# Optimization experiments

Measured on AMD Instinct MI355X. Metric: run time of the kernel, lower is better.

## Reference

```python
import jax, jax.numpy as jnp
import numpy as np

H = 8
D_MODEL = 1024
D_K = D_MODEL // H
NEG = -1000000000.0


def layer_norm(x, a, b, eps=1e-06):
    # torch std: unbiased (ddof=1); module divides by (std + eps)
    mean = jnp.mean(x, axis=-1, keepdims=True)
    var = jnp.sum((x - mean) ** 2, axis=-1, keepdims=True) / (x.shape[-1] - 1)
    std = jnp.sqrt(var)
    return a * (x - mean) / (std + eps) + b


def setup_inputs() -> dict:
    key = jax.random.key(0)
    ks = jax.random.split(key, 12)
    B, S, D = 8, 1024, D_MODEL
    inp = {
        "query": jax.random.normal(ks[0], (B, S, D), jnp.float32),
        "value": jax.random.normal(ks[1], (B, S, D), jnp.float32),
        "key": jax.random.normal(ks[2], (B, S, D), jnp.float32),
        "mask": jax.random.randint(ks[3], (B, S), 0, 2, jnp.int32),
        "ln_a": jnp.ones((D,), jnp.float32),
        "ln_b": jnp.zeros((D,), jnp.float32),
        "wq": jax.random.normal(ks[4], (D, D), jnp.float32) * 0.02,
        "bq": jnp.zeros((D,), jnp.float32),
        "wk": jax.random.normal(ks[5], (D, D), jnp.float32) * 0.02,
        "bk": jnp.zeros((D,), jnp.float32),
        "wv": jax.random.normal(ks[6], (D, D), jnp.float32) * 0.02,
        "bv": jnp.zeros((D,), jnp.float32),
        "w_aoa": jax.random.normal(ks[7], (2 * D, 2 * D), jnp.float32) * 0.02,  # [out, in]
        "b_aoa": jnp.zeros((2 * D,), jnp.float32),
    }
    return inp


def reference(query, value, key, mask, ln_a, ln_b, wq, bq, wk, bk, wv, bv, w_aoa, b_aoa):
    B, S, D = query.shape
    # mask [B,S] -> [B,1,1,S]
    m = mask[:, None, None, :]
    # norm_q
    q = layer_norm(query, ln_a, ln_b)
    # QKV projections, split heads -> [B,H,S,Dk]
    def split_heads(x):
        return x.reshape(B, -1, H, D_K).transpose(0, 2, 1, 3)
    q_ = split_heads(q @ wq.T + bq)
    k_ = split_heads(key @ wk.T + bk)
    v_ = split_heads(value @ wv.T + bv)
    scores = jnp.einsum("bhqd,bhkd->bhqk", q_, k_) / jnp.sqrt(jnp.float32(D_K))
    scores = jnp.where(m == 0, NEG, scores)
    p = jax.nn.softmax(scores, axis=-1)
    x = jnp.einsum("bhqk,bhkd->bhqd", p, v_)
    x = x.transpose(0, 2, 1, 3).reshape(B, S, D)
    # AoA: concat with (normed) query, linear to 2D, GLU
    z = jnp.concatenate([x, q], axis=-1) @ w_aoa.T + b_aoa
    a, g = jnp.split(z, 2, axis=-1)
    return a * jax.nn.sigmoid(g)
```

## Files before the change

### kernel.cpp

```cpp
#include <hip/hip_runtime.h>

typedef __attribute__((ext_vector_type(8))) __bf16 bf16x8;
typedef __attribute__((ext_vector_type(4))) float f32x4;

__device__ __forceinline__ ushort f2b(float f) {
    uint u = __builtin_bit_cast(uint, f);
    u += 0x7fffu + ((u >> 16) & 1u);
    return (ushort)(u >> 16);
}
__device__ __forceinline__ float b2f(ushort h) {
    uint u = ((uint)h) << 16;
    return __builtin_bit_cast(float, u);
}

__global__ __launch_bounds__(256) void cast_kernel(const float* __restrict__ src,
                                                   ushort* __restrict__ dst) {
    size_t i = ((size_t)blockIdx.x * 256 + threadIdx.x) * 4;
    float4 v = *(const float4*)(src + i);
    ushort4 o;
    o.x = f2b(v.x); o.y = f2b(v.y); o.z = f2b(v.z); o.w = f2b(v.w);
    *(ushort4*)(dst + i) = o;
}

__global__ __launch_bounds__(256) void cast_permute_aoa(const float* __restrict__ src,
                                                        ushort* __restrict__ dst) {
    int n1 = blockIdx.x >> 1;
    int c = (blockIdx.x & 1) * 1024 + threadIdx.x * 4;
    int q = ((n1 & 63) | ((n1 >> 7) << 6)) + ((n1 >> 6) & 1) * 1024;
    float4 v = *(const float4*)(src + (size_t)q * 2048 + c);
    ushort4 o;
    o.x = f2b(v.x); o.y = f2b(v.y); o.z = f2b(v.z); o.w = f2b(v.w);
    *(ushort4*)(dst + (size_t)n1 * 2048 + c) = o;
}

__global__ __launch_bounds__(256) void ln_kernel(const float* __restrict__ x,
                                                 const float* __restrict__ ga,
                                                 const float* __restrict__ be,
                                                 ushort* __restrict__ xq) {
    const int row = blockIdx.x, tid = threadIdx.x;
    __shared__ float red[4];
    float4 v = ((const float4*)(x + (size_t)row * 1024))[tid];
    float sm = v.x + v.y + v.z + v.w;
    for (int off = 32; off; off >>= 1) sm += __shfl_xor(sm, off);
    if ((tid & 63) == 0) red[tid >> 6] = sm;
    __syncthreads();
    float mean = (red[0] + red[1] + red[2] + red[3]) * (1.f / 1024.f);
    __syncthreads();
    float dx = v.x - mean, dy = v.y - mean, dz = v.z - mean, dw = v.w - mean;
    float s2 = dx * dx + dy * dy + dz * dz + dw * dw;
    for (int off = 32; off; off >>= 1) s2 += __shfl_xor(s2, off);
    if ((tid & 63) == 0) red[tid >> 6] = s2;
    __syncthreads();
    float var = (red[0] + red[1] + red[2] + red[3]) * (1.f / 1023.f);
    float inv = 1.f / (sqrtf(var) + 1e-6f);
    float4 g = ((const float4*)ga)[tid];
    float4 bb = ((const float4*)be)[tid];
    ushort4 o;
    o.x = f2b(g.x * dx * inv + bb.x);
    o.y = f2b(g.y * dy * inv + bb.y);
    o.z = f2b(g.z * dz * inv + bb.z);
    o.w = f2b(g.w * dw * inv + bb.w);
    *(ushort4*)&xq[(size_t)row * 2048 + 1024 + tid * 4] = o;
}

template <int MODE>
__global__ __launch_bounds__(512, 2) void gemm4(const ushort* __restrict__ Aq, int ldaq,
                                                const ushort* __restrict__ Ak,
                                                const ushort* __restrict__ Av,
                                                const ushort* __restrict__ B, int ldb,
                                                const float* __restrict__ bias0,
                                                const float* __restrict__ bias1,
                                                const float* __restrict__ bias2,
                                                void* __restrict__ out0,
                                                void* __restrict__ out1,
                                                void* __restrict__ out2,
                                                int K, int NB, float qscale) {
    __shared__ ushort lds[2][32768];

    const int tid = threadIdx.x;
    const int w = tid >> 6, l = tid & 63;
    const int wr = w >> 2, wcn = w & 3;
    const int r16 = l & 15, g4 = l >> 4;

    const int bid = blockIdx.x;
    const int cpx = gridDim.x >> 3;
    const int swz = (bid & 7) * cpx + (bid >> 3);
    const int m0 = (swz / NB) * 256;
    const int n0 = (swz % NB) * 256;

    const int region = (MODE == 0) ? (n0 >> 10) : 0;
    const ushort* A = (MODE == 0) ? (region == 0 ? Aq : (region == 1 ? Ak : Av)) : Aq;
    const int lda = (MODE == 0) ? (region == 0 ? ldaq : 1024) : ldaq;

    const int srow8 = l >> 3;
    const int sxor8 = ((l & 7) ^ srow8) * 8;
    const ushort* As0 = A + (size_t)(m0 + w * 8 + srow8) * lda + sxor8;
    const ushort* Bs0 = B + (size_t)(n0 + w * 8 + srow8) * ldb + sxor8;

    f32x4 acc[8][4];
#pragma unroll
    for (int i = 0; i < 8; i++)
#pragma unroll
        for (int j = 0; j < 4; j++) acc[i][j] = (f32x4){0.f, 0.f, 0.f, 0.f};

    const int sw16 = (r16 & 7) << 4;
    char* ldsb = (char*)&lds[0][0];

#define GL16(src_, dst_)                                                        \
    __builtin_amdgcn_global_load_lds(                                           \
        (const __attribute__((address_space(1))) void*)(src_),                  \
        (__attribute__((address_space(3))) void*)(dst_), 16, 0, 0)

    auto STAGE8 = [&](int sel, int kt) {
        const size_t ko = (size_t)kt * 64;
#pragma unroll
        for (int li = 0; li < 2; li++)
            GL16(As0 + (size_t)(li * 64) * lda + ko,
                 ldsb + sel * 65536 + li * 8192 + w * 1024);
#pragma unroll
        for (int li = 0; li < 2; li++)
            GL16(Bs0 + (size_t)(li * 64) * ldb + ko,
                 ldsb + sel * 65536 + 32768 + li * 8192 + w * 1024);
#pragma unroll
        for (int li = 0; li < 2; li++)
            GL16(As0 + (size_t)(128 + li * 64) * lda + ko,
                 ldsb + sel * 65536 + 16384 + li * 8192 + w * 1024);
#pragma unroll
        for (int li = 0; li < 2; li++)
            GL16(Bs0 + (size_t)(128 + li * 64) * ldb + ko,
                 ldsb + sel * 65536 + 32768 + 16384 + li * 8192 + w * 1024);
    };

    auto LDA4 = [&](bf16x8 (&dst)[4][2], int sel, int half) {
#pragma unroll
        for (int ai = 0; ai < 4; ai++)
#pragma unroll
            for (int ks = 0; ks < 2; ks++)
                dst[ai][ks] = *(const bf16x8*)(ldsb + sel * 65536 + half * 16384 +
                                               (wr * 16 + 32 * ai + r16) * 128 +
                                               ((ks * 64 + g4 * 16) ^ sw16));
    };
    auto LDB2 = [&](bf16x8 (&dst)[2][2], int sel, int half) {
#pragma unroll
        for (int bi = 0; bi < 2; bi++)
#pragma unroll
            for (int ks = 0; ks < 2; ks++)
                dst[bi][ks] = *(const bf16x8*)(ldsb + sel * 65536 + 32768 + half * 16384 +
                                               (wcn * 16 + 64 * bi + r16) * 128 +
                                               ((ks * 64 + g4 * 16) ^ sw16));
    };
    auto MM = [&](bf16x8 (&af)[4][2], bf16x8 (&bf)[2][2], int A0, int B0) {
        __builtin_amdgcn_s_setprio(1);
#pragma unroll
        for (int ks = 0; ks < 2; ks++)
#pragma unroll
            for (int ai = 0; ai < 4; ai++)
#pragma unroll
                for (int bi = 0; bi < 2; bi++)
                    acc[A0 + ai][B0 + bi] = __builtin_amdgcn_mfma_f32_16x16x32_bf16(
                        af[ai][ks], bf[bi][ks], acc[A0 + ai][B0 + bi], 0, 0, 0);
        __builtin_amdgcn_s_setprio(0);
    };

    const int NT = K >> 6;

    STAGE8(0, 0);
    asm volatile("s_waitcnt vmcnt(0)" ::: "memory");
    __builtin_amdgcn_s_barrier();

    bf16x8 aL[4][2], aH[4][2], bL[2][2], bH[2][2];

    for (int t = 0; t < NT - 1; ++t) {
        const int sel = t & 1;
        LDA4(aL, sel, 0); LDB2(bL, sel, 0);
        STAGE8(sel ^ 1, t + 1);
        __builtin_amdgcn_s_barrier();
        MM(aL, bL, 0, 0);
        asm volatile("s_waitcnt vmcnt(8)" ::: "memory");
        __builtin_amdgcn_s_barrier();
        LDA4(aH, sel, 1);
        __builtin_amdgcn_s_barrier();
        MM(aH, bL, 4, 0);
        __builtin_amdgcn_s_barrier();
        LDB2(bH, sel, 1);
        __builtin_amdgcn_s_barrier();
        MM(aH, bH, 4, 2);
        __builtin_amdgcn_s_barrier();
        MM(aL, bH, 0, 2);
        asm volatile("s_waitcnt vmcnt(4)" ::: "memory");
        __builtin_amdgcn_s_barrier();
    }
    {
        const int sel = (NT - 1) & 1;
        LDA4(aL, sel, 0); LDB2(bL, sel, 0);
        __builtin_amdgcn_s_barrier();
        MM(aL, bL, 0, 0);
        asm volatile("s_waitcnt vmcnt(0)" ::: "memory");
        __builtin_amdgcn_s_barrier();
        LDA4(aH, sel, 1);
        LDB2(bH, sel, 1);
        MM(aH, bL, 4, 0);
        MM(aH, bH, 4, 2);
        MM(aL, bH, 0, 2);
    }
#undef GL16

    if (MODE == 1) {
        float* out = (float*)out0;
#pragma unroll
        for (int bp = 0; bp < 2; bp++) {
            int j = (n0 >> 1) + wcn * 16 + 64 * bp + r16;
            float bsa = bias0[j];
            float bsg = bias0[j + 1024];
#pragma unroll
            for (int a_ = 0; a_ < 8; a_++) {
                int mr = m0 + wr * 16 + 32 * a_ + g4 * 4;
#pragma unroll
                for (int r = 0; r < 4; r++) {
                    float av = acc[a_][2 * bp][r] + bsa;
                    float gv = acc[a_][2 * bp + 1][r] + bsg;
                    out[(size_t)(mr + r) * 1024 + j] = av * (1.f / (1.f + __expf(-gv)));
                }
            }
        }
    } else {
        const int nr0 = n0 & 1023;
        const float* bias = region == 0 ? bias0 : (region == 1 ? bias1 : bias2);
        const float scale = region == 0 ? qscale : 1.f;
        if (region < 2) {
            ushort* C = (ushort*)(region == 0 ? out0 : out1);
#pragma unroll
            for (int b_ = 0; b_ < 4; b_++) {
                int n = nr0 + wcn * 16 + 64 * b_ + r16;
                float bs = bias[n];
#pragma unroll
                for (int a_ = 0; a_ < 8; a_++) {
                    int mr = m0 + wr * 16 + 32 * a_ + g4 * 4;
#pragma unroll
                    for (int r = 0; r < 4; r++)
                        C[(size_t)(mr + r) * 1024 + n] = f2b((acc[a_][b_][r] + bs) * scale);
                }
            }
        } else {
            ushort* Vt = (ushort*)out2;
#pragma unroll
            for (int b_ = 0; b_ < 4; b_++) {
                int n = nr0 + wcn * 16 + 64 * b_ + r16;
                float bs = bias[n];
                int h = n >> 7, d = n & 127;
#pragma unroll
                for (int a_ = 0; a_ < 8; a_++) {
                    int mr = m0 + wr * 16 + 32 * a_ + g4 * 4;
                    int bb = mr >> 10, s_ = mr & 1023;
                    ushort4 o;
                    o.x = f2b(acc[a_][b_][0] + bs);
                    o.y = f2b(acc[a_][b_][1] + bs);
                    o.z = f2b(acc[a_][b_][2] + bs);
                    o.w = f2b(acc[a_][b_][3] + bs);
                    *(ushort4*)&Vt[((size_t)(bb * 8 + h) * 128 + d) * 1024 + s_] = o;
                }
            }
        }
    }
}

__global__ __launch_bounds__(512, 4) void attn_kernel(const ushort* __restrict__ Q,
                                                      const ushort* __restrict__ Kt,
                                                      const ushort* __restrict__ Vt,
                                                      const int* __restrict__ mask,
                                                      ushort* __restrict__ xq) {
    __shared__ ushort Ks[2][8192];
    __shared__ ushort Vs[2][8192];
    __shared__ ushort Pl[8][1024];

    const int tid = threadIdx.x;
    const int l = tid & 63, wid = tid >> 6;
    const int r16 = l & 15, g4 = l >> 4;
    const int id = blockIdx.x;
    const int bh = ((id >> 6) << 3) | (id & 7);
    const int qb = (id >> 3) & 7;
    const int b = bh >> 3, h = bh & 7;
    const int q0 = qb * 128 + wid * 16;

    bf16x8 qf[4];
    const ushort* Qrow = Q + (size_t)(b * 1024 + q0 + r16) * 1024 + h * 128 + g4 * 8;
#pragma unroll
    for (int kf = 0; kf < 4; kf++) qf[kf] = *(const bf16x8*)(Qrow + kf * 32);

    const ushort* Kg = Kt + ((size_t)b * 1024) * 1024 + h * 128;
    const ushort* Vg = Vt + (size_t)(b * 8 + h) * 128 * 1024;
    const int* mptr = mask + b * 1024;

    f32x4 xacc[8];
#pragma unroll
    for (int i = 0; i < 8; i++) xacc[i] = (f32x4){0.f, 0.f, 0.f, 0.f};
    float mrow = -INFINITY, lrow = 0.f, sclp = 0.f;

    char* Pme = (char*)&Pl[wid][0];
    const int pswz = (r16 & 7) << 4;

    auto STAGE_K = [&](int sel, int t) {
        const int kv0 = t * 64;
#pragma unroll
        for (int it = 0; it < 2; ++it) {
            int ob = it * 8192 + wid * 1024;
            int o = ob + l * 16;
            int row = o >> 8;
            int sc = (o & 255) ^ ((row & 7) << 4);
            const ushort* src = Kg + (size_t)(kv0 + row) * 1024 + (sc >> 1);
            __builtin_amdgcn_global_load_lds((const __attribute__((address_space(1))) void*)src,
                (__attribute__((address_space(3))) void*)((char*)&Ks[sel][0] + ob), 16, 0, 0);
        }
    };
    auto STAGE_V = [&](int sel, int t) {
        const int kv0 = t * 64;
#pragma unroll
        for (int it = 0; it < 2; ++it) {
            int ob = it * 8192 + wid * 1024;
            int o = ob + l * 16;
            int d = o >> 7;
            int sc = (o & 127) ^ ((d & 7) << 4);
            const ushort* src = Vg + (size_t)d * 1024 + kv0 + (sc >> 1);
            __builtin_amdgcn_global_load_lds((const __attribute__((address_space(1))) void*)src,
                (__attribute__((address_space(3))) void*)((char*)&Vs[sel][0] + ob), 16, 0, 0);
        }
    };

    auto QK = [&](f32x4 (&s)[4], int sel, unsigned long long wt) {
        const char* Kb_ = (const char*)&Ks[sel][0];
#pragma unroll
        for (int cg = 0; cg < 4; cg++) {
            s[cg] = (f32x4){0.f, 0.f, 0.f, 0.f};
            const int rowk = cg * 16 + r16;
            const char* kr = Kb_ + rowk * 256;
            const int sw = (rowk & 7) << 4;
            __builtin_amdgcn_s_setprio(1);
#pragma unroll
            for (int kf = 0; kf < 4; kf++) {
                bf16x8 kfr = *(const bf16x8*)(kr + ((kf * 64 + g4 * 16) ^ sw));
                s[cg] = __builtin_amdgcn_mfma_f32_16x16x32_bf16(kfr, qf[kf], s[cg], 0, 0, 0);
            }
            __builtin_amdgcn_s_setprio(0);
            uint nib = (uint)(wt >> (cg * 16 + g4 * 4)) & 15u;
#pragma unroll
            for (int r = 0; r < 4; r++)
                if (!((nib >> r) & 1u)) s[cg][r] = -1e9f;
        }
    };
    auto PV = [&](int sel) {
        const char* Vb_ = (const char*)&Vs[sel][0];
        bf16x8 pfr[2];
#pragma unroll
        for (int ks = 0; ks < 2; ks++)
            pfr[ks] = *(const bf16x8*)(Pme + r16 * 128 + ((g4 * 16 + ks * 64) ^ pswz));
#pragma unroll
        for (int cg2 = 0; cg2 < 8; cg2++)
#pragma unroll
            for (int r = 0; r < 4; r++) xacc[cg2][r] *= sclp;
        __builtin_amdgcn_s_setprio(1);
#pragma unroll
        for (int ks = 0; ks < 2; ks++) {
#pragma unroll
            for (int cg2 = 0; cg2 < 8; cg2++) {
                const int d = cg2 * 16 + r16;
                bf16x8 vfr = *(const bf16x8*)(Vb_ + d * 128 + ((ks * 64 + g4 * 16) ^ ((d & 7) << 4)));
                xacc[cg2] = __builtin_amdgcn_mfma_f32_16x16x32_bf16(vfr, pfr[ks], xacc[cg2], 0, 0, 0);
            }
        }
        __builtin_amdgcn_s_setprio(0);
    };
    auto SOFTMAX = [&](f32x4 (&s)[4]) {
        float pmax = -INFINITY;
#pragma unroll
        for (int cg = 0; cg < 4; cg++)
#pragma unroll
            for (int r = 0; r < 4; r++) pmax = fmaxf(pmax, s[cg][r]);
        pmax = fmaxf(pmax, __shfl_xor(pmax, 16));
        pmax = fmaxf(pmax, __shfl_xor(pmax, 32));
        float mn = fmaxf(mrow, pmax);
        sclp = __expf(mrow - mn);
        mrow = mn;
        float rsum = 0.f;
#pragma unroll
        for (int cg = 0; cg < 4; cg++)
#pragma unroll
            for (int r = 0; r < 4; r++) {
                float p = __expf(s[cg][r] - mn);
                s[cg][r] = p;
                rsum += p;
            }
        rsum += __shfl_xor(rsum, 16);
        rsum += __shfl_xor(rsum, 32);
        lrow = lrow * sclp + rsum;
#pragma unroll
        for (int cg = 0; cg < 4; cg++) {
            uint lo = ((uint)f2b(s[cg][1]) << 16) | f2b(s[cg][0]);
            uint hi = ((uint)f2b(s[cg][3]) << 16) | f2b(s[cg][2]);
            uint2 pk; pk.x = lo; pk.y = hi;
            *(uint2*)(Pme + r16 * 128 + ((cg * 32 + g4 * 8) ^ pswz)) = pk;
        }
    };

    STAGE_K(0, 0);
    int mv = mptr[l];
    asm volatile("s_waitcnt vmcnt(0)" ::: "memory");
    __syncthreads();
    STAGE_K(1, 1);
    STAGE_V(0, 0);
    unsigned long long wt = __ballot(mv != 0);
    mv = mptr[64 + l];
    {
        f32x4 s0[4];
        QK(s0, 0, wt);
        SOFTMAX(s0);
    }
    int kc = 1, vc = 0;

    for (int u = 1; u < 16; ++u) {
        wt = __ballot(mv != 0);
        asm volatile("s_waitcnt vmcnt(0)" ::: "memory");
        __syncthreads();
        if (u < 15) STAGE_K(kc ^ 1, u + 1);
        STAGE_V(vc ^ 1, u);
        if (u < 15) mv = mptr[(u + 1) * 64 + l];

        f32x4 sn[4];
        QK(sn, kc, wt);
        PV(vc);
        SOFTMAX(sn);

        kc ^= 1; vc ^= 1;
    }

    asm volatile("s_waitcnt vmcnt(0)" ::: "memory");
    __syncthreads();
    PV(vc);

    const float inv = 1.f / lrow;
    const size_t orow = (size_t)(b * 1024 + q0 + r16) * 2048 + h * 128;
#pragma unroll
    for (int cg2 = 0; cg2 < 8; cg2++) {
#pragma unroll
        for (int r = 0; r < 4; r++) {
            xq[orow + cg2 * 16 + g4 * 4 + r] = f2b(xacc[cg2][r] * inv);
        }
    }
}

extern "C" void kernel_launch(void* const* d_in, const int* in_sizes, int n_in,
                              void* d_out, int out_size, void* d_ws, size_t ws_size,
                              hipStream_t stream) {
    const float* query = (const float*)d_in[0];
    const float* value = (const float*)d_in[1];
    const float* key   = (const float*)d_in[2];
    const int*   mask  = (const int*)d_in[3];
    const float* ln_a  = (const float*)d_in[4];
    const float* ln_b  = (const float*)d_in[5];
    const float* wq    = (const float*)d_in[6];
    const float* bq    = (const float*)d_in[7];
    const float* wk    = (const float*)d_in[8];
    const float* bk    = (const float*)d_in[9];
    const float* wv    = (const float*)d_in[10];
    const float* bv    = (const float*)d_in[11];
    const float* waoa  = (const float*)d_in[12];
    const float* baoa  = (const float*)d_in[13];
    float* out = (float*)d_out;

    char* w8 = (char*)d_ws;
    ushort* xq   = (ushort*)(w8);
    ushort* Qb   = (ushort*)(w8 + 33554432);
    ushort* Kb   = (ushort*)(w8 + 50331648);
    ushort* Vt   = (ushort*)(w8 + 67108864);
    ushort* keyb = (ushort*)(w8 + 83886080);
    ushort* valb = (ushort*)(w8 + 100663296);
    ushort* wqb  = (ushort*)(w8 + 117440512);
    ushort* wkb  = (ushort*)(w8 + 119537664);
    ushort* wvb  = (ushort*)(w8 + 121634816);
    ushort* wab  = (ushort*)(w8 + 123731968);

    cast_kernel<<<8192, 256, 0, stream>>>(key, keyb);
    cast_kernel<<<8192, 256, 0, stream>>>(value, valb);
    cast_kernel<<<1024, 256, 0, stream>>>(wq, wqb);
    cast_kernel<<<1024, 256, 0, stream>>>(wk, wkb);
    cast_kernel<<<1024, 256, 0, stream>>>(wv, wvb);
    cast_permute_aoa<<<4096, 256, 0, stream>>>(waoa, wab);
    ln_kernel<<<8192, 256, 0, stream>>>(query, ln_a, ln_b, xq);

    const float qscale = 0.08838834764831845f;

    gemm4<0><<<384, 512, 0, stream>>>(xq + 1024, 2048, keyb, valb,
                                      wqb, 1024, bq, bk, bv,
                                      Qb, Kb, Vt, 1024, 12, qscale);

    attn_kernel<<<512, 512, 0, stream>>>(Qb, Kb, Vt, mask, xq);

    gemm4<1><<<256, 512, 0, stream>>>(xq, 2048, nullptr, nullptr,
                                      wab, 2048, baoa, nullptr, nullptr,
                                      out, nullptr, nullptr, 2048, 8, 1.f);
}
```

Before: 241.4 us.

## Split GEMM prefetch into quarter stages interleaved with MFMA phases

```diff
diff --git a/kernel.cpp b/kernel.cpp
--- a/kernel.cpp
+++ b/kernel.cpp
@@ -64,7 +64,7 @@
 }
 
 template <int MODE>
-__global__ __launch_bounds__(512, 2) void gemm4(const ushort* __restrict__ Aq, int ldaq,
+__global__ __launch_bounds__(512, 2) void gemm5(const ushort* __restrict__ Aq, int ldaq,
                                                 const ushort* __restrict__ Ak,
                                                 const ushort* __restrict__ Av,
                                                 const ushort* __restrict__ B, int ldb,
@@ -106,30 +106,19 @@
     const int sw16 = (r16 & 7) << 4;
     char* ldsb = (char*)&lds[0][0];
 
-#define GL16(src_, dst_)                                                        \
-    __builtin_amdgcn_global_load_lds(                                           \
-        (const __attribute__((address_space(1))) void*)(src_),                  \
-        (__attribute__((address_space(3))) void*)(dst_), 16, 0, 0)
-
-    auto STAGE8 = [&](int sel, int kt) {
-        const size_t ko = (size_t)kt * 64;
-#pragma unroll
-        for (int li = 0; li < 2; li++)
-            GL16(As0 + (size_t)(li * 64) * lda + ko,
-                 ldsb + sel * 65536 + li * 8192 + w * 1024);
-#pragma unroll
-        for (int li = 0; li < 2; li++)
-            GL16(Bs0 + (size_t)(li * 64) * ldb + ko,
-                 ldsb + sel * 65536 + 32768 + li * 8192 + w * 1024);
-#pragma unroll
-        for (int li = 0; li < 2; li++)
-            GL16(As0 + (size_t)(128 + li * 64) * lda + ko,
-                 ldsb + sel * 65536 + 16384 + li * 8192 + w * 1024);
-#pragma unroll
-        for (int li = 0; li < 2; li++)
-            GL16(Bs0 + (size_t)(128 + li * 64) * ldb + ko,
-                 ldsb + sel * 65536 + 32768 + 16384 + li * 8192 + w * 1024);
-    };
+#define STAGE_H(sel_, HS_, kt_)                                                            \
+    do {                                                                                   \
+        const int mat_ = (HS_)&1, half_ = (HS_) >> 1;                                      \
+        const ushort* sb_ = mat_ ? Bs0 : As0;                                              \
+        const int ld_ = mat_ ? ldb : lda;                                                  \
+        _Pragma("unroll") for (int li_ = 0; li_ < 2; li_++) {                              \
+            const ushort* src_ = sb_ + (size_t)(half_ * 128 + li_ * 64) * ld_ + (kt_)*64;  \
+            int dst_ = (sel_)*65536 + mat_ * 32768 + half_ * 16384 + li_ * 8192 + w * 1024;\
+            __builtin_amdgcn_global_load_lds(                                              \
+                (const __attribute__((address_space(1))) void*)src_,                       \
+                (__attribute__((address_space(3))) void*)(ldsb + dst_), 16, 0, 0);         \
+        }                                                                                  \
+    } while (0)
 
     auto LDA4 = [&](bf16x8 (&dst)[4][2], int sel, int half) {
 #pragma unroll
@@ -164,46 +153,40 @@
 
     const int NT = K >> 6;
 
-    STAGE8(0, 0);
+    STAGE_H(0, 0, 0); STAGE_H(0, 1, 0); STAGE_H(0, 2, 0); STAGE_H(0, 3, 0);
     asm volatile("s_waitcnt vmcnt(0)" ::: "memory");
     __builtin_amdgcn_s_barrier();
 
     bf16x8 aL[4][2], aH[4][2], bL[2][2], bH[2][2];
 
-    for (int t = 0; t < NT - 1; ++t) {
+    for (int t = 0; t < NT; ++t) {
         const int sel = t & 1;
+        const bool pf = (t + 1 < NT);
         LDA4(aL, sel, 0); LDB2(bL, sel, 0);
-        STAGE8(sel ^ 1, t + 1);
+        if (pf) STAGE_H(sel ^ 1, 0, t + 1);
         __builtin_amdgcn_s_barrier();
         MM(aL, bL, 0, 0);
-        asm volatile("s_waitcnt vmcnt(8)" ::: "memory");
+        asm volatile("s_waitcnt vmcnt(4)" ::: "memory");
         __builtin_amdgcn_s_barrier();
         LDA4(aH, sel, 1);
+        if (pf) STAGE_H(sel ^ 1, 1, t + 1);
         __builtin_amdgcn_s_barrier();
         MM(aH, bL, 4, 0);
+        asm volatile("s_waitcnt vmcnt(4)" ::: "memory");
         __builtin_amdgcn_s_barrier();
         LDB2(bH, sel, 1);
+        if (pf) STAGE_H(sel ^ 1, 2, t + 1);
         __builtin_amdgcn_s_barrier();
         MM(aH, bH, 4, 2);
+        asm volatile("s_waitcnt vmcnt(4)" ::: "memory");
+        __builtin_amdgcn_s_barrier();
+        if (pf) STAGE_H(sel ^ 1, 3, t + 1);
         __builtin_amdgcn_s_barrier();
         MM(aL, bH, 0, 2);
         asm volatile("s_waitcnt vmcnt(4)" ::: "memory");
         __builtin_amdgcn_s_barrier();
     }
-    {
-        const int sel = (NT - 1) & 1;
-        LDA4(aL, sel, 0); LDB2(bL, sel, 0);
-        __builtin_amdgcn_s_barrier();
-        MM(aL, bL, 0, 0);
-        asm volatile("s_waitcnt vmcnt(0)" ::: "memory");
-        __builtin_amdgcn_s_barrier();
-        LDA4(aH, sel, 1);
-        LDB2(bH, sel, 1);
-        MM(aH, bL, 4, 0);
-        MM(aH, bH, 4, 2);
-        MM(aL, bH, 0, 2);
-    }
-#undef GL16
+#undef STAGE_H
 
     if (MODE == 1) {
         float* out = (float*)out0;
@@ -488,13 +471,13 @@
 
     const float qscale = 0.08838834764831845f;
 
-    gemm4<0><<<384, 512, 0, stream>>>(xq + 1024, 2048, keyb, valb,
+    gemm5<0><<<384, 512, 0, stream>>>(xq + 1024, 2048, keyb, valb,
                                       wqb, 1024, bq, bk, bv,
                                       Qb, Kb, Vt, 1024, 12, qscale);
 
     attn_kernel<<<512, 512, 0, stream>>>(Qb, Kb, Vt, mask, xq);
 
-    gemm4<1><<<256, 512, 0, stream>>>(xq, 2048, nullptr, nullptr,
+    gemm5<1><<<256, 512, 0, stream>>>(xq, 2048, nullptr, nullptr,
                                       wab, 2048, baoa, nullptr, nullptr,
                                       out, nullptr, nullptr, 2048, 8, 1.f);
 }
```

Result: no change. 243.7 us (+0.9%).
